# Kernel optimization log

Hardware: AMD Instinct MI355X
Metric: run time of the kernel (lower is better)

The kernel has to match this reference:

```python
import jax, jax.numpy as jnp
import numpy as np
import math

N_NODES = 8192
DEG = 32            # fixed neighbors per node (edges grouped by destination)
EMBED = 256
NHEAD = 8
HDIM = EMBED // NHEAD
E = N_NODES * DEG


def setup_inputs() -> dict:
    key = jax.random.key(0)
    ks = jax.random.split(key, 8)
    feats = jax.random.normal(ks[0], (N_NODES, EMBED), dtype=jnp.float32)
    # edge_index[:,0] = source (random), edge_index[:,1] = destination, grouped so
    # that edges [i*DEG:(i+1)*DEG] all have destination i (required by the
    # 'h (n a) d -> h n a d' rearrange in the original module).
    src = jax.random.randint(ks[1], (E,), 0, N_NODES, dtype=jnp.int32)
    dst = jnp.repeat(jnp.arange(N_NODES, dtype=jnp.int32), DEG)
    edge_index = jnp.stack([src, dst], axis=1)
    edge_attr = jnp.zeros((E,), dtype=jnp.float32)  # unused (mult_attr=0)
    xav = math.sqrt(2.0 / (EMBED + EMBED))  # xavier_uniform ~ this scale
    def lin_w(k):
        return jax.random.uniform(k, (EMBED, EMBED), jnp.float32, -1.0, 1.0) * xav * math.sqrt(3.0)
    return {
        "feats": feats,
        "edge_index": edge_index,
        "edge_attr": edge_attr,
        "Wq": lin_w(ks[2]), "bq": jnp.zeros((EMBED,), jnp.float32),
        "Wk": lin_w(ks[3]), "bk": jnp.zeros((EMBED,), jnp.float32),
        "Wv": lin_w(ks[4]), "bv": jnp.zeros((EMBED,), jnp.float32),
        "Wo": lin_w(ks[5]), "bo": jnp.zeros((EMBED,), jnp.float32),
    }


def reference(feats, edge_index, edge_attr, Wq, bq, Wk, bk, Wv, bv, Wo, bo):
    n = feats.shape[0]
    e = edge_index.shape[0]
    a = e // n  # neighbors per node
    # projections, split into heads: (h, n, d)
    def proj(W, b):
        return (feats @ W.T + b).reshape(n, NHEAD, HDIM).transpose(1, 0, 2)
    q, k, v = proj(Wq, bq), proj(Wk, bk), proj(Wv, bv)
    r = edge_index[:, 0]  # source nodes -> keys/values
    c = edge_index[:, 1]  # destination nodes -> queries
    qe = q[:, c, :].reshape(NHEAD, n, a, HDIM)
    ke = k[:, r, :].reshape(NHEAD, n, a, HDIM)
    ve = v[:, r, :].reshape(NHEAD, n, a, HDIM)
    sim = jnp.einsum('hnad,hnad->hna', qe, ke) / math.sqrt(HDIM)
    attn = jax.nn.softmax(sim, axis=-1)  # softmax over neighbors
    out = jnp.einsum('hna,hnad->hnd', attn, ve)  # (h, n, d)
    out = out.transpose(1, 0, 2).reshape(n, EMBED)  # n (h d)
    return out @ Wo.T + bo
```

## Files before the change

### kernel.cpp

```cpp
#include <hip/hip_runtime.h>
#include <hip/hip_bf16.h>
#include <math.h>

#define N_NODES 8192
#define DEG 32
#define EMBED 256
#define NHEAD 8
#define HDIM 32

typedef __attribute__((ext_vector_type(8))) short bf16x8;
typedef __attribute__((ext_vector_type(8))) unsigned short ushort8;
typedef __attribute__((ext_vector_type(4))) float f32x4;

__device__ __forceinline__ unsigned short f2bf(float x) {
    union { float f; unsigned int u; } c; c.f = x;
    unsigned int r = (c.u + 0x7FFFu + ((c.u >> 16) & 1u)) >> 16;
    return (unsigned short)r;
}
__device__ __forceinline__ float bf2f(unsigned short u) {
    union { unsigned int u; float f; } c; c.u = ((unsigned int)u) << 16;
    return c.f;
}

__global__ __launch_bounds__(256) void convert_all(
        const float* __restrict__ feats,
        const float* __restrict__ Wq, const float* __restrict__ Wk,
        const float* __restrict__ Wv, const float* __restrict__ Wo,
        const float* __restrict__ bq, const float* __restrict__ bk,
        const float* __restrict__ bv,
        unsigned short* __restrict__ Xb,
        unsigned short* __restrict__ Wqkvb, unsigned short* __restrict__ Wob,
        float* __restrict__ bias768) {
    const int b = blockIdx.x;
    if (b < 2048) {
        const int i = (b * 256 + threadIdx.x) * 4;
        const float4 v = *reinterpret_cast<const float4*>(&feats[i]);
        ushort4 r;
        r.x = f2bf(v.x); r.y = f2bf(v.y); r.z = f2bf(v.z); r.w = f2bf(v.w);
        *reinterpret_cast<ushort4*>(&Xb[i]) = r;
    } else if (b < 2304) {
        const int bb  = b - 2048;
        const int seg = bb >> 6;
        const int i = (bb & 63) * 1024 + threadIdx.x * 4;
        const float* src = (seg == 0) ? Wq : (seg == 1) ? Wk : (seg == 2) ? Wv : Wo;
        const float4 v = *reinterpret_cast<const float4*>(&src[i]);
        ushort4 r;
        r.x = f2bf(v.x); r.y = f2bf(v.y); r.z = f2bf(v.z); r.w = f2bf(v.w);
        if (seg < 3) *reinterpret_cast<ushort4*>(&Wqkvb[seg * 65536 + i]) = r;
        else         *reinterpret_cast<ushort4*>(&Wob[i]) = r;
    } else {
        const int i = threadIdx.x;
        bias768[i]       = bq[i];
        bias768[256 + i] = bk[i];
        bias768[512 + i] = bv[i];
    }
}

template <int IS_QKV>
__global__ __launch_bounds__(256) void gemm_mfma(const unsigned short* __restrict__ X,
                                                 const unsigned short* __restrict__ W,
                                                 const float* __restrict__ bias,
                                                 float* __restrict__ outF,
                                                 unsigned short* __restrict__ outKV) {
    __shared__ unsigned short Xs[64][72];
    __shared__ unsigned short Ws[64][72];
    const int t    = threadIdx.x;
    const int bm   = blockIdx.y * 64;
    const int bn   = blockIdx.x * 64;
    const int lane = t & 63;
    const int wv   = t >> 6;
    const int wm   = (wv >> 1) * 32;
    const int wn   = (wv & 1) * 32;
    const int fr   = lane & 15;
    const int ksel = lane >> 4;

    f32x4 acc[2][2] = {};

    for (int k0 = 0; k0 < 256; k0 += 64) {
#pragma unroll
        for (int i = 0; i < 2; ++i) {
            const int id  = i * 256 + t;
            const int row = id >> 3;
            const int c   = id & 7;
            *reinterpret_cast<uint4*>(&Xs[row][c * 8]) =
                *reinterpret_cast<const uint4*>(&X[(bm + row) * 256 + k0 + c * 8]);
            *reinterpret_cast<uint4*>(&Ws[row][c * 8]) =
                *reinterpret_cast<const uint4*>(&W[(bn + row) * 256 + k0 + c * 8]);
        }
        __syncthreads();
#pragma unroll
        for (int kf = 0; kf < 2; ++kf) {
            const int ck = (kf * 4 + ksel) * 8;
            bf16x8 a0 = *reinterpret_cast<const bf16x8*>(&Xs[wm + fr][ck]);
            bf16x8 a1 = *reinterpret_cast<const bf16x8*>(&Xs[wm + 16 + fr][ck]);
            bf16x8 b0 = *reinterpret_cast<const bf16x8*>(&Ws[wn + fr][ck]);
            bf16x8 b1 = *reinterpret_cast<const bf16x8*>(&Ws[wn + 16 + fr][ck]);
            acc[0][0] = __builtin_amdgcn_mfma_f32_16x16x32_bf16(a0, b0, acc[0][0], 0, 0, 0);
            acc[0][1] = __builtin_amdgcn_mfma_f32_16x16x32_bf16(a0, b1, acc[0][1], 0, 0, 0);
            acc[1][0] = __builtin_amdgcn_mfma_f32_16x16x32_bf16(a1, b0, acc[1][0], 0, 0, 0);
            acc[1][1] = __builtin_amdgcn_mfma_f32_16x16x32_bf16(a1, b1, acc[1][1], 0, 0, 0);
        }
        __syncthreads();
    }

#pragma unroll
    for (int mf = 0; mf < 2; ++mf)
#pragma unroll
        for (int nf = 0; nf < 2; ++nf)
#pragma unroll
            for (int reg = 0; reg < 4; ++reg) {
                const int row = bm + wm + mf * 16 + ksel * 4 + reg;
                const int col = bn + wn + nf * 16 + fr;
                const float v = acc[mf][nf][reg] + bias[col];
                if (IS_QKV) {
                    if (col < 256) outF[row * 256 + col] = v;
                    else           outKV[row * 512 + (col - 256)] = f2bf(v);
                } else {
                    outF[row * 256 + col] = v;
                }
            }
}

__global__ __launch_bounds__(256) void edge_attn(const float* __restrict__ Qf,
                                                 const unsigned short* __restrict__ KVb,
                                                 const int* __restrict__ edge_index,
                                                 unsigned short* __restrict__ attb) {
    const int n = blockIdx.x;
    const int t = threadIdx.x;
    const int h = t >> 5;
    const int j = t & 31;
    __shared__ int   s_src[DEG];
    __shared__ float Qs[EMBED];
    __shared__ float wls[NHEAD][DEG];

    if (t < DEG) s_src[t] = edge_index[(n * DEG + t) * 2];
    Qs[t] = Qf[n * EMBED + t];
    __syncthreads();

    const unsigned short* kp = &KVb[(size_t)s_src[j] * 512 + h * HDIM];
    float s = 0.f;
#pragma unroll
    for (int c = 0; c < 4; ++c) {
        const ushort8 kv = *reinterpret_cast<const ushort8*>(&kp[c * 8]);
        const float4 q0 = *reinterpret_cast<const float4*>(&Qs[h * HDIM + c * 8]);
        const float4 q1 = *reinterpret_cast<const float4*>(&Qs[h * HDIM + c * 8 + 4]);
        s = fmaf(bf2f(kv[0]), q0.x, s);
        s = fmaf(bf2f(kv[1]), q0.y, s);
        s = fmaf(bf2f(kv[2]), q0.z, s);
        s = fmaf(bf2f(kv[3]), q0.w, s);
        s = fmaf(bf2f(kv[4]), q1.x, s);
        s = fmaf(bf2f(kv[5]), q1.y, s);
        s = fmaf(bf2f(kv[6]), q1.z, s);
        s = fmaf(bf2f(kv[7]), q1.w, s);
    }
    s *= 0.17677669529663687f;

    float m = s;
    m = fmaxf(m, __shfl_xor(m, 1));
    m = fmaxf(m, __shfl_xor(m, 2));
    m = fmaxf(m, __shfl_xor(m, 4));
    m = fmaxf(m, __shfl_xor(m, 8));
    m = fmaxf(m, __shfl_xor(m, 16));
    const float p = __expf(s - m);
    float den = p;
    den += __shfl_xor(den, 1);
    den += __shfl_xor(den, 2);
    den += __shfl_xor(den, 4);
    den += __shfl_xor(den, 8);
    den += __shfl_xor(den, 16);
    wls[h][j] = p / den;
    __syncthreads();

    float o = 0.f;
#pragma unroll
    for (int jj = 0; jj < DEG; ++jj) {
        o = fmaf(wls[h][jj],
                 bf2f(KVb[(size_t)s_src[jj] * 512 + 256 + h * HDIM + j]), o);
    }
    attb[n * EMBED + t] = f2bf(o);
}

extern "C" void kernel_launch(void* const* d_in, const int* in_sizes, int n_in,
                              void* d_out, int out_size, void* d_ws, size_t ws_size,
                              hipStream_t stream) {
    const float* feats      = (const float*)d_in[0];
    const int*   edge_index = (const int*)d_in[1];
    const float* Wq = (const float*)d_in[3];
    const float* bq = (const float*)d_in[4];
    const float* Wk = (const float*)d_in[5];
    const float* bk = (const float*)d_in[6];
    const float* Wv = (const float*)d_in[7];
    const float* bv = (const float*)d_in[8];
    const float* Wo = (const float*)d_in[9];
    const float* bo = (const float*)d_in[10];
    float* out = (float*)d_out;

    unsigned short* Xb     = (unsigned short*)d_ws;
    unsigned short* Wqkvb  = Xb + 8192 * 256;
    unsigned short* Wob    = Wqkvb + 768 * 256;
    float*          bias768= (float*)(Wob + 256 * 256);
    float*          Qf     = (float*)((char*)bias768 + 4096);
    unsigned short* KVb    = (unsigned short*)(Qf + 8192 * 256);
    unsigned short* attb   = KVb + (size_t)8192 * 512;

    convert_all<<<2305, 256, 0, stream>>>(feats, Wq, Wk, Wv, Wo, bq, bk, bv,
                                          Xb, Wqkvb, Wob, bias768);
    gemm_mfma<1><<<dim3(12, 128), 256, 0, stream>>>(Xb, Wqkvb, bias768, Qf, KVb);
    edge_attn<<<N_NODES, 256, 0, stream>>>(Qf, KVb, edge_index, attb);
    gemm_mfma<0><<<dim3(4, 128), 256, 0, stream>>>(attb, Wob, bo, out, nullptr);
}
```

Before: 128.4 us.

## Fuse fp32-to-bf16 conversion of inputs and weights into the GEMM tile loads

Removes the separate conversion kernel and converts feats and weight tiles from fp32 to bf16 while staging them into shared memory inside the GEMMs. Bias is read straight from the original per-projection arrays. This drops one kernel launch and the round trip of writing then rereading bf16 copies. In exchange, each GEMM block reads fp32 data (twice the bytes) and feats is re-converted by all 12 column blocks.

```diff
diff --git a/kernel.cpp b/kernel.cpp
--- a/kernel.cpp
+++ b/kernel.cpp
@@ -22,46 +22,15 @@
     return c.f;
 }
 
-__global__ __launch_bounds__(256) void convert_all(
-        const float* __restrict__ feats,
-        const float* __restrict__ Wq, const float* __restrict__ Wk,
-        const float* __restrict__ Wv, const float* __restrict__ Wo,
-        const float* __restrict__ bq, const float* __restrict__ bk,
-        const float* __restrict__ bv,
-        unsigned short* __restrict__ Xb,
-        unsigned short* __restrict__ Wqkvb, unsigned short* __restrict__ Wob,
-        float* __restrict__ bias768) {
-    const int b = blockIdx.x;
-    if (b < 2048) {
-        const int i = (b * 256 + threadIdx.x) * 4;
-        const float4 v = *reinterpret_cast<const float4*>(&feats[i]);
-        ushort4 r;
-        r.x = f2bf(v.x); r.y = f2bf(v.y); r.z = f2bf(v.z); r.w = f2bf(v.w);
-        *reinterpret_cast<ushort4*>(&Xb[i]) = r;
-    } else if (b < 2304) {
-        const int bb  = b - 2048;
-        const int seg = bb >> 6;
-        const int i = (bb & 63) * 1024 + threadIdx.x * 4;
-        const float* src = (seg == 0) ? Wq : (seg == 1) ? Wk : (seg == 2) ? Wv : Wo;
-        const float4 v = *reinterpret_cast<const float4*>(&src[i]);
-        ushort4 r;
-        r.x = f2bf(v.x); r.y = f2bf(v.y); r.z = f2bf(v.z); r.w = f2bf(v.w);
-        if (seg < 3) *reinterpret_cast<ushort4*>(&Wqkvb[seg * 65536 + i]) = r;
-        else         *reinterpret_cast<ushort4*>(&Wob[i]) = r;
-    } else {
-        const int i = threadIdx.x;
-        bias768[i]       = bq[i];
-        bias768[256 + i] = bk[i];
-        bias768[512 + i] = bv[i];
-    }
-}
-
 template <int IS_QKV>
-__global__ __launch_bounds__(256) void gemm_mfma(const unsigned short* __restrict__ X,
-                                                 const unsigned short* __restrict__ W,
-                                                 const float* __restrict__ bias,
-                                                 float* __restrict__ outF,
-                                                 unsigned short* __restrict__ outKV) {
+__global__ __launch_bounds__(256) void gemm_fused(
+        const float* __restrict__ Xf,
+        const unsigned short* __restrict__ Xb16,
+        const float* __restrict__ W0, const float* __restrict__ W1,
+        const float* __restrict__ W2,
+        const float* __restrict__ b0, const float* __restrict__ b1,
+        const float* __restrict__ b2,
+        float* __restrict__ outF, unsigned short* __restrict__ outKV) {
     __shared__ unsigned short Xs[64][72];
     __shared__ unsigned short Ws[64][72];
     const int t    = threadIdx.x;
@@ -74,18 +43,46 @@
     const int fr   = lane & 15;
     const int ksel = lane >> 4;
 
+    const int seg = IS_QKV ? (int)(blockIdx.x >> 2) : 0;
+    const float* wsrc = (seg == 0) ? W0 : (seg == 1) ? W1 : W2;
+    const float* bsrc = (seg == 0) ? b0 : (seg == 1) ? b1 : b2;
+    const int wr0 = (IS_QKV ? (int)(blockIdx.x & 3) : (int)blockIdx.x) * 64;
+
     f32x4 acc[2][2] = {};
 
     for (int k0 = 0; k0 < 256; k0 += 64) {
-#pragma unroll
-        for (int i = 0; i < 2; ++i) {
+        if (IS_QKV) {
+#pragma unroll
+            for (int i = 0; i < 4; ++i) {
+                const int id  = i * 256 + t;
+                const int row = id >> 4;
+                const int c4  = (id & 15) * 4;
+                const float4 v = *reinterpret_cast<const float4*>(
+                    &Xf[(bm + row) * 256 + k0 + c4]);
+                ushort4 r;
+                r.x = f2bf(v.x); r.y = f2bf(v.y); r.z = f2bf(v.z); r.w = f2bf(v.w);
+                *reinterpret_cast<ushort4*>(&Xs[row][c4]) = r;
+            }
+        } else {
+#pragma unroll
+            for (int i = 0; i < 2; ++i) {
+                const int id  = i * 256 + t;
+                const int row = id >> 3;
+                const int c   = (id & 7) * 8;
+                *reinterpret_cast<uint4*>(&Xs[row][c]) =
+                    *reinterpret_cast<const uint4*>(&Xb16[(bm + row) * 256 + k0 + c]);
+            }
+        }
+#pragma unroll
+        for (int i = 0; i < 4; ++i) {
             const int id  = i * 256 + t;
-            const int row = id >> 3;
-            const int c   = id & 7;
-            *reinterpret_cast<uint4*>(&Xs[row][c * 8]) =
-                *reinterpret_cast<const uint4*>(&X[(bm + row) * 256 + k0 + c * 8]);
-            *reinterpret_cast<uint4*>(&Ws[row][c * 8]) =
-                *reinterpret_cast<const uint4*>(&W[(bn + row) * 256 + k0 + c * 8]);
+            const int row = id >> 4;
+            const int c4  = (id & 15) * 4;
+            const float4 v = *reinterpret_cast<const float4*>(
+                &wsrc[(wr0 + row) * 256 + k0 + c4]);
+            ushort4 r;
+            r.x = f2bf(v.x); r.y = f2bf(v.y); r.z = f2bf(v.z); r.w = f2bf(v.w);
+            *reinterpret_cast<ushort4*>(&Ws[row][c4]) = r;
         }
         __syncthreads();
 #pragma unroll
@@ -93,12 +90,12 @@
             const int ck = (kf * 4 + ksel) * 8;
             bf16x8 a0 = *reinterpret_cast<const bf16x8*>(&Xs[wm + fr][ck]);
             bf16x8 a1 = *reinterpret_cast<const bf16x8*>(&Xs[wm + 16 + fr][ck]);
-            bf16x8 b0 = *reinterpret_cast<const bf16x8*>(&Ws[wn + fr][ck]);
-            bf16x8 b1 = *reinterpret_cast<const bf16x8*>(&Ws[wn + 16 + fr][ck]);
-            acc[0][0] = __builtin_amdgcn_mfma_f32_16x16x32_bf16(a0, b0, acc[0][0], 0, 0, 0);
-            acc[0][1] = __builtin_amdgcn_mfma_f32_16x16x32_bf16(a0, b1, acc[0][1], 0, 0, 0);
-            acc[1][0] = __builtin_amdgcn_mfma_f32_16x16x32_bf16(a1, b0, acc[1][0], 0, 0, 0);
-            acc[1][1] = __builtin_amdgcn_mfma_f32_16x16x32_bf16(a1, b1, acc[1][1], 0, 0, 0);
+            bf16x8 b0v = *reinterpret_cast<const bf16x8*>(&Ws[wn + fr][ck]);
+            bf16x8 b1v = *reinterpret_cast<const bf16x8*>(&Ws[wn + 16 + fr][ck]);
+            acc[0][0] = __builtin_amdgcn_mfma_f32_16x16x32_bf16(a0, b0v, acc[0][0], 0, 0, 0);
+            acc[0][1] = __builtin_amdgcn_mfma_f32_16x16x32_bf16(a0, b1v, acc[0][1], 0, 0, 0);
+            acc[1][0] = __builtin_amdgcn_mfma_f32_16x16x32_bf16(a1, b0v, acc[1][0], 0, 0, 0);
+            acc[1][1] = __builtin_amdgcn_mfma_f32_16x16x32_bf16(a1, b1v, acc[1][1], 0, 0, 0);
         }
         __syncthreads();
     }
@@ -111,7 +108,7 @@
             for (int reg = 0; reg < 4; ++reg) {
                 const int row = bm + wm + mf * 16 + ksel * 4 + reg;
                 const int col = bn + wn + nf * 16 + fr;
-                const float v = acc[mf][nf][reg] + bias[col];
+                const float v = acc[mf][nf][reg] + bsrc[col & 255];
                 if (IS_QKV) {
                     if (col < 256) outF[row * 256 + col] = v;
                     else           outKV[row * 512 + (col - 256)] = f2bf(v);
@@ -195,17 +192,15 @@
     const float* bo = (const float*)d_in[10];
     float* out = (float*)d_out;
 
-    unsigned short* Xb     = (unsigned short*)d_ws;
-    unsigned short* Wqkvb  = Xb + 8192 * 256;
-    unsigned short* Wob    = Wqkvb + 768 * 256;
-    float*          bias768= (float*)(Wob + 256 * 256);
-    float*          Qf     = (float*)((char*)bias768 + 4096);
-    unsigned short* KVb    = (unsigned short*)(Qf + 8192 * 256);
-    unsigned short* attb   = KVb + (size_t)8192 * 512;
-
-    convert_all<<<2305, 256, 0, stream>>>(feats, Wq, Wk, Wv, Wo, bq, bk, bv,
-                                          Xb, Wqkvb, Wob, bias768);
-    gemm_mfma<1><<<dim3(12, 128), 256, 0, stream>>>(Xb, Wqkvb, bias768, Qf, KVb);
+    float*          Qf   = (float*)d_ws;
+    unsigned short* KVb  = (unsigned short*)(Qf + (size_t)8192 * 256);
+    unsigned short* attb = KVb + (size_t)8192 * 512;
+
+    gemm_fused<1><<<dim3(12, 128), 256, 0, stream>>>(feats, nullptr,
+                                                     Wq, Wk, Wv, bq, bk, bv,
+                                                     Qf, KVb);
     edge_attn<<<N_NODES, 256, 0, stream>>>(Qf, KVb, edge_index, attb);
-    gemm_mfma<0><<<dim3(4, 128), 256, 0, stream>>>(attb, Wob, bo, out, nullptr);
-}
+    gemm_fused<0><<<dim3(4, 128), 256, 0, stream>>>(nullptr, attb,
+                                                    Wo, Wo, Wo, bo, bo, bo,
+                                                    out, nullptr);
+}
```

Measured after the change: 130.8 us. About the same (+1.8%).
